# Optimization experiments

Hardware: AMD Instinct MI355X
Metric: run time of the kernel (lower is better)

Reference implementation:

```python
import jax, jax.numpy as jnp
import numpy as np

B, T, C, H = 4, 2048, 1024, 16
D = C // H  # head_size = 64


def setup_inputs() -> dict:
    key = jax.random.key(0)
    k1, k2, k3 = jax.random.split(key, 3)
    x = jax.random.normal(k1, (B, T, C), dtype=jnp.float32)
    w_qkv = jax.random.normal(k2, (C, 3 * C), dtype=jnp.float32) * (C ** -0.5)
    b_qkv = jnp.zeros((3 * C,), dtype=jnp.float32)
    w_proj = jax.random.normal(k3, (C, C), dtype=jnp.float32) * (C ** -0.5)
    b_proj = jnp.zeros((C,), dtype=jnp.float32)
    return {"x": x, "w_qkv": w_qkv, "b_qkv": b_qkv, "w_proj": w_proj, "b_proj": b_proj}


def reference(x, w_qkv, b_qkv, w_proj, b_proj):
    b, t, c = x.shape
    qkv = x @ w_qkv + b_qkv                      # [B,T,3C]
    q, k, v = jnp.split(qkv, 3, axis=-1)
    # [B,T,C] -> [B,H,T,D]
    q = q.reshape(b, t, H, D).transpose(0, 2, 1, 3)
    k = k.reshape(b, t, H, D).transpose(0, 2, 1, 3)
    v = v.reshape(b, t, H, D).transpose(0, 2, 1, 3)
    attn = jnp.einsum('bhqd,bhkd->bhqk', q, k) * (D ** -0.5)
    causal = jnp.tril(jnp.ones((t, t), dtype=bool))
    attn = jnp.where(causal[None, None], attn, -jnp.inf)
    attn = jax.nn.softmax(attn, axis=-1)
    # dropout: eval mode (identity)
    out = jnp.einsum('bhqk,bhkd->bhqd', attn, v)
    out = out.transpose(0, 2, 1, 3).reshape(b, t, c)
    return out @ w_proj + b_proj
```

## Files before the change

kernel.cpp:

```cpp
#include <hip/hip_runtime.h>

#define B_ 4
#define T_ 2048
#define C_ 1024
#define H_ 16
#define D_ 64

typedef __attribute__((ext_vector_type(8))) short short8;
typedef __attribute__((ext_vector_type(4))) float f32x4;

__device__ inline unsigned short f2bf(float f) {
    union { float f; unsigned u; } v; v.f = f;
    unsigned r = v.u + 0x7fffu + ((v.u >> 16) & 1u);
    return (unsigned short)(r >> 16);
}

__device__ inline unsigned int pk_bf16(float a, float b) {
#if __has_builtin(__builtin_amdgcn_cvt_pk_bf16_f32)
    typedef __attribute__((ext_vector_type(2))) __bf16 bf16x2;
    bf16x2 v = __builtin_amdgcn_cvt_pk_bf16_f32(a, b);
    return __builtin_bit_cast(unsigned int, v);
#else
    return (unsigned)f2bf(a) | ((unsigned)f2bf(b) << 16);
#endif
}

__device__ inline void async_ld16(const void* g, void* lds) {
    __builtin_amdgcn_global_load_lds(
        (const __attribute__((address_space(1))) unsigned int*)g,
        (__attribute__((address_space(3))) unsigned int*)lds, 16, 0, 0);
}

__global__ __launch_bounds__(256) void prep_all(
    const float* __restrict__ x, const float* __restrict__ w_qkv,
    const float* __restrict__ w_proj,
    unsigned short* __restrict__ xb, unsigned short* __restrict__ wqkvT,
    unsigned short* __restrict__ wprojT)
{
    const int bid = blockIdx.x;
    if (bid < 8192) {
        int i = (bid * 256 + threadIdx.x) * 4;
        float4 v = *(const float4*)(x + i);
        uint2 o;
        o.x = pk_bf16(v.x, v.y);
        o.y = pk_bf16(v.z, v.w);
        *(uint2*)(xb + i) = o;
        return;
    }
    __shared__ float tile[32][33];
    const int tt = bid - 8192;
    int bx = tt & 127;
    const int by = tt >> 7;
    const float* src; unsigned short* dst; int Cc;
    if (bx < 96) { src = w_qkv;  dst = wqkvT;  Cc = 3072; }
    else         { src = w_proj; dst = wprojT; Cc = 1024; bx -= 96; }
    const int tx = threadIdx.x & 31, ty = threadIdx.x >> 5;
    #pragma unroll
    for (int r = 0; r < 32; r += 8)
        tile[ty + r][tx] = src[(size_t)(by*32 + ty + r) * Cc + bx*32 + tx];
    __syncthreads();
    #pragma unroll
    for (int r = 0; r < 32; r += 8)
        dst[(size_t)(bx*32 + ty + r) * 1024 + by*32 + tx] = f2bf(tile[tx][ty + r]);
}

__global__ __launch_bounds__(256) void gemm_qkv(
    const unsigned short* __restrict__ A,
    const unsigned short* __restrict__ BT,
    const float* __restrict__ bias,
    unsigned short* __restrict__ qb, unsigned short* __restrict__ kb,
    unsigned short* __restrict__ vtb)
{
    __shared__ unsigned short As0[128 * 32], As1[128 * 32];
    __shared__ unsigned short Bs0[128 * 32], Bs1[128 * 32];
    const int tid = threadIdx.x;
    const int wave = tid >> 6, lane = tid & 63;
    const int wm = wave >> 1, wn = wave & 1;
    const int l15 = lane & 15, lq = lane >> 4;
    const int m0 = blockIdx.y * 128, n0 = blockIdx.x * 128;
    const int srow = tid >> 2, sg = tid & 3;
    const int sel = n0 >> 10;

    f32x4 acc[4][4] = {};

    for (int k0 = 0; k0 < 1024; k0 += 64) {
        #pragma unroll
        for (int r = 0; r < 2; ++r) {
            const size_t ra = (size_t)(m0 + r*64 + srow) * 1024 + k0 + sg*8;
            const size_t rb = (size_t)(n0 + r*64 + srow) * 1024 + k0 + sg*8;
            async_ld16(A  + ra,      (char*)As0 + r*4096 + wave*1024);
            async_ld16(A  + ra + 32, (char*)As1 + r*4096 + wave*1024);
            async_ld16(BT + rb,      (char*)Bs0 + r*4096 + wave*1024);
            async_ld16(BT + rb + 32, (char*)Bs1 + r*4096 + wave*1024);
        }
        __syncthreads();
        #pragma unroll
        for (int ks = 0; ks < 2; ++ks) {
            const unsigned short* Asx = ks ? As1 : As0;
            const unsigned short* Bsx = ks ? Bs1 : Bs0;
            short8 af[4], bf[4];
            #pragma unroll
            for (int i = 0; i < 4; ++i) {
                af[i] = *(const short8*)&Asx[(wm*64 + i*16 + l15) * 32 + lq*8];
                bf[i] = *(const short8*)&Bsx[(wn*64 + i*16 + l15) * 32 + lq*8];
            }
            if (sel < 2) {
                #pragma unroll
                for (int mi = 0; mi < 4; ++mi)
                    #pragma unroll
                    for (int ni = 0; ni < 4; ++ni)
                        acc[mi][ni] = __builtin_amdgcn_mfma_f32_16x16x32_bf16(
                            bf[ni], af[mi], acc[mi][ni], 0, 0, 0);
            } else {
                #pragma unroll
                for (int mi = 0; mi < 4; ++mi)
                    #pragma unroll
                    for (int ni = 0; ni < 4; ++ni)
                        acc[mi][ni] = __builtin_amdgcn_mfma_f32_16x16x32_bf16(
                            af[mi], bf[ni], acc[mi][ni], 0, 0, 0);
            }
        }
        __syncthreads();
    }

    if (sel < 2) {
        const float qs = (sel == 0) ? 0.180336880f : 1.0f;
        unsigned short* dst = (sel == 0) ? qb : kb;
        #pragma unroll
        for (int mi = 0; mi < 4; ++mi) {
            const int t = m0 + wm*64 + mi*16 + l15;
            const int bb = t >> 11, tt = t & 2047;
            #pragma unroll
            for (int ni = 0; ni < 4; ++ni) {
                const int nb = n0 + wn*64 + ni*16 + lq*4;
                const int hh = (nb >> 6) & 15, d0 = nb & 63;
                float4 bv = *(const float4*)(bias + nb);
                float v0 = (acc[mi][ni][0] + bv.x) * qs;
                float v1 = (acc[mi][ni][1] + bv.y) * qs;
                float v2 = (acc[mi][ni][2] + bv.z) * qs;
                float v3 = (acc[mi][ni][3] + bv.w) * qs;
                uint2 pk; pk.x = pk_bf16(v0, v1); pk.y = pk_bf16(v2, v3);
                *(uint2*)(dst + ((size_t)(bb*16 + hh)*2048 + tt)*64 + d0) = pk;
            }
        }
    } else {
        #pragma unroll
        for (int mi = 0; mi < 4; ++mi) {
            const int t0 = m0 + wm*64 + mi*16 + lq*4;
            const int bb = t0 >> 11, tt = t0 & 2047;
            const int tl = tt & 63;
            const int tp = (tt & ~63) | (tl & 32) | ((tl & 12) << 1) | ((tl & 16) >> 2);
            #pragma unroll
            for (int ni = 0; ni < 4; ++ni) {
                const int n = n0 + wn*64 + ni*16 + l15;
                const int hh = (n >> 6) & 15, d = n & 63;
                const float bs = bias[n];
                uint2 pk;
                pk.x = pk_bf16(acc[mi][ni][0] + bs, acc[mi][ni][1] + bs);
                pk.y = pk_bf16(acc[mi][ni][2] + bs, acc[mi][ni][3] + bs);
                *(uint2*)(vtb + ((size_t)(bb*16 + hh)*64 + d)*2048 + tp) = pk;
            }
        }
    }
}

__global__ __launch_bounds__(256) void gemm_proj(
    const unsigned short* __restrict__ A,
    const unsigned short* __restrict__ BT,
    const float* __restrict__ bias,
    float* __restrict__ out)
{
    __shared__ unsigned short As0[128 * 32], As1[128 * 32];
    __shared__ unsigned short Bs0[128 * 32], Bs1[128 * 32];
    const int tid = threadIdx.x;
    const int wave = tid >> 6, lane = tid & 63;
    const int wm = wave >> 1, wn = wave & 1;
    const int l15 = lane & 15, lq = lane >> 4;
    const int m0 = blockIdx.y * 128, n0 = blockIdx.x * 128;
    const int srow = tid >> 2, sg = tid & 3;

    f32x4 acc[4][4] = {};

    for (int k0 = 0; k0 < 1024; k0 += 64) {
        #pragma unroll
        for (int r = 0; r < 2; ++r) {
            const size_t ra = (size_t)(m0 + r*64 + srow) * 1024 + k0 + sg*8;
            const size_t rb = (size_t)(n0 + r*64 + srow) * 1024 + k0 + sg*8;
            async_ld16(A  + ra,      (char*)As0 + r*4096 + wave*1024);
            async_ld16(A  + ra + 32, (char*)As1 + r*4096 + wave*1024);
            async_ld16(BT + rb,      (char*)Bs0 + r*4096 + wave*1024);
            async_ld16(BT + rb + 32, (char*)Bs1 + r*4096 + wave*1024);
        }
        __syncthreads();
        #pragma unroll
        for (int ks = 0; ks < 2; ++ks) {
            const unsigned short* Asx = ks ? As1 : As0;
            const unsigned short* Bsx = ks ? Bs1 : Bs0;
            short8 af[4], bf[4];
            #pragma unroll
            for (int i = 0; i < 4; ++i) {
                af[i] = *(const short8*)&Asx[(wm*64 + i*16 + l15) * 32 + lq*8];
                bf[i] = *(const short8*)&Bsx[(wn*64 + i*16 + l15) * 32 + lq*8];
            }
            #pragma unroll
            for (int mi = 0; mi < 4; ++mi)
                #pragma unroll
                for (int ni = 0; ni < 4; ++ni)
                    acc[mi][ni] = __builtin_amdgcn_mfma_f32_16x16x32_bf16(
                        bf[ni], af[mi], acc[mi][ni], 0, 0, 0);
        }
        __syncthreads();
    }

    #pragma unroll
    for (int mi = 0; mi < 4; ++mi) {
        const int m = m0 + wm*64 + mi*16 + l15;
        #pragma unroll
        for (int ni = 0; ni < 4; ++ni) {
            const int nb = n0 + wn*64 + ni*16 + lq*4;
            float4 bv = *(const float4*)(bias + nb);
            float4 o;
            o.x = acc[mi][ni][0] + bv.x;
            o.y = acc[mi][ni][1] + bv.y;
            o.z = acc[mi][ni][2] + bv.z;
            o.w = acc[mi][ni][3] + bv.w;
            *(float4*)(out + (size_t)m * 1024 + nb) = o;
        }
    }
}

__global__ __launch_bounds__(256, 2) void attn_mfma(
    const unsigned short* __restrict__ qb,
    const unsigned short* __restrict__ kb,
    const unsigned short* __restrict__ vtb,
    unsigned short* __restrict__ ab)
{
    extern __shared__ unsigned char smem[];
    const int tid  = threadIdx.x;
    const int wave = tid >> 6, lane = tid & 63;
    const int l15  = lane & 15, lq = lane >> 4;
    const int linear = blockIdx.x;
    const int xc  = linear & 7;
    const int idx = linear >> 3;
    const int bh  = xc * 8 + (idx & 7);
    const int qblk = 31 - (idx >> 3);
    const int q0 = qblk * 64;
    const int b = bh >> 4, h = bh & 15;
    const size_t base = (size_t)bh * 2048 * 64;

    unsigned short* Kw = (unsigned short*)(smem + wave * 16384);
    unsigned short* Vw = Kw + 4096;

    const int row8 = lane >> 3;
    const int chx8 = ((lane & 7) ^ row8) * 8;

#define STAGE_K(J0) do { _Pragma("unroll") for (int op = 0; op < 8; ++op) \
    async_ld16(kb + base + (size_t)((J0) + op*8 + row8)*64 + chx8, \
               (char*)Kw + op*1024); } while (0)
#define STAGE_V(J0) do { _Pragma("unroll") for (int op = 0; op < 8; ++op) \
    async_ld16(vtb + base + (size_t)(op*8 + row8)*2048 + (J0) + chx8, \
               (char*)Vw + op*1024); } while (0)

    short8 qf[2][4];
    #pragma unroll
    for (int ks = 0; ks < 2; ++ks)
        #pragma unroll
        for (int nq = 0; nq < 4; ++nq)
            qf[ks][nq] = *(const short8*)(qb + base
                + (size_t)(q0 + nq*16 + l15)*64 + ks*32 + lq*8);

    f32x4 o[4][4] = {};
    float lacc[4] = {0.f, 0.f, 0.f, 0.f};

    const int jfirst = wave * 64;
    const int nt = (qblk >= wave) ? ((qblk - wave) >> 2) + 1 : 0;

    if (nt > 0) { STAGE_K(jfirst); STAGE_V(jfirst); }

    for (int i = 0; i < nt; ++i) {
        const int j0 = jfirst + i * 256;
        const bool more = (i + 1 < nt);

        asm volatile("s_waitcnt vmcnt(8)" ::: "memory");

        short8 kf0[4], kf1[4];
        #pragma unroll
        for (int ni = 0; ni < 4; ++ni) {
            const unsigned short* kr = Kw + (ni*16 + l15) * 64;
            kf0[ni] = *(const short8*)(kr + (((0*4 + lq) ^ (l15 & 7)) << 3));
            kf1[ni] = *(const short8*)(kr + (((1*4 + lq) ^ (l15 & 7)) << 3));
        }
        f32x4 s[4][4] = {};
        #pragma unroll
        for (int ni = 0; ni < 4; ++ni)
            #pragma unroll
            for (int nq = 0; nq < 4; ++nq) {
                s[ni][nq] = __builtin_amdgcn_mfma_f32_16x16x32_bf16(
                    kf0[ni], qf[0][nq], s[ni][nq], 0, 0, 0);
                s[ni][nq] = __builtin_amdgcn_mfma_f32_16x16x32_bf16(
                    kf1[ni], qf[1][nq], s[ni][nq], 0, 0, 0);
            }
        asm volatile("s_waitcnt lgkmcnt(0)" ::: "memory");
        if (more) STAGE_K(j0 + 256);

        if (j0 == q0) {
            #pragma unroll
            for (int ni = 0; ni < 4; ++ni)
                #pragma unroll
                for (int nq = 0; nq < 4; ++nq)
                    #pragma unroll
                    for (int r = 0; r < 4; ++r)
                        if (ni*16 + lq*4 + r > nq*16 + l15)
                            s[ni][nq][r] = -1e30f;
        }

        short8 pf[2][4];
        #pragma unroll
        for (int c = 0; c < 2; ++c)
            #pragma unroll
            for (int nq = 0; nq < 4; ++nq) {
                float p0 = __builtin_amdgcn_exp2f(s[2*c  ][nq][0]);
                float p1 = __builtin_amdgcn_exp2f(s[2*c  ][nq][1]);
                float p2 = __builtin_amdgcn_exp2f(s[2*c  ][nq][2]);
                float p3 = __builtin_amdgcn_exp2f(s[2*c  ][nq][3]);
                float p4 = __builtin_amdgcn_exp2f(s[2*c+1][nq][0]);
                float p5 = __builtin_amdgcn_exp2f(s[2*c+1][nq][1]);
                float p6 = __builtin_amdgcn_exp2f(s[2*c+1][nq][2]);
                float p7 = __builtin_amdgcn_exp2f(s[2*c+1][nq][3]);
                lacc[nq] += ((p0 + p1) + (p2 + p3)) + ((p4 + p5) + (p6 + p7));
                uint4 pu;
                pu.x = pk_bf16(p0, p1); pu.y = pk_bf16(p2, p3);
                pu.z = pk_bf16(p4, p5); pu.w = pk_bf16(p6, p7);
                pf[c][nq] = __builtin_bit_cast(short8, pu);
            }

        if (more) asm volatile("s_waitcnt vmcnt(8)" ::: "memory");
        else      asm volatile("s_waitcnt vmcnt(0)" ::: "memory");

        #pragma unroll
        for (int c = 0; c < 2; ++c) {
            short8 vf[4];
            #pragma unroll
            for (int nd = 0; nd < 4; ++nd)
                vf[nd] = *(const short8*)(Vw + (nd*16 + l15) * 64
                    + (((c*4 + lq) ^ (l15 & 7)) << 3));
            #pragma unroll
            for (int nq = 0; nq < 4; ++nq)
                #pragma unroll
                for (int nd = 0; nd < 4; ++nd)
                    o[nq][nd] = __builtin_amdgcn_mfma_f32_16x16x32_bf16(
                        pf[c][nq], vf[nd], o[nq][nd], 0, 0, 0);
        }
        asm volatile("s_waitcnt lgkmcnt(0)" ::: "memory");
        if (more) STAGE_V(j0 + 256);
    }
#undef STAGE_K
#undef STAGE_V

    #pragma unroll
    for (int nq = 0; nq < 4; ++nq) {
        float t = lacc[nq];
        t += __shfl_xor(t, 16);
        t += __shfl_xor(t, 32);
        if (lq == 0) ((float*)Kw)[nq*16 + l15] = t;
    }
    __syncthreads();
    const int qg = wave, d = lane;
    f32x4 linv4[4];
    #pragma unroll
    for (int j = 0; j < 4; ++j) {
        f32x4 lsum = {};
        #pragma unroll
        for (int w2 = 0; w2 < 4; ++w2)
            lsum += *(const f32x4*)((const float*)(smem + w2*16384) + qg*16 + j*4);
        #pragma unroll
        for (int r = 0; r < 4; ++r)
            linv4[j][r] = __builtin_amdgcn_rcpf(lsum[r]);
    }
    __syncthreads();
    #pragma unroll
    for (int nq = 0; nq < 4; ++nq)
        #pragma unroll
        for (int nd = 0; nd < 4; ++nd) {
            const int row = nd*16 + l15;
            const int col = (nq*16 + lq*4 + 4*l15) & 63;
            *(f32x4*)((float*)Kw + row*64 + col) = o[nq][nd];
        }
    __syncthreads();
    #pragma unroll
    for (int j = 0; j < 4; ++j) {
        const int colb = (qg*16 + j*4 + 4*(d & 15)) & 63;
        f32x4 acc = {};
        #pragma unroll
        for (int w2 = 0; w2 < 4; ++w2)
            acc += *(const f32x4*)((const float*)(smem + w2*16384) + d*64 + colb);
        #pragma unroll
        for (int r = 0; r < 4; ++r) {
            const int q = qg*16 + j*4 + r;
            ab[(size_t)(b*2048 + q0 + q)*1024 + h*64 + d] = f2bf(acc[r] * linv4[j][r]);
        }
    }
}

extern "C" void kernel_launch(void* const* d_in, const int* in_sizes, int n_in,
                              void* d_out, int out_size, void* d_ws, size_t ws_size,
                              hipStream_t stream) {
    const float* x      = (const float*)d_in[0];
    const float* w_qkv  = (const float*)d_in[1];
    const float* b_qkv  = (const float*)d_in[2];
    const float* w_proj = (const float*)d_in[3];
    const float* b_proj = (const float*)d_in[4];
    float* out = (float*)d_out;

    unsigned short* xb     = (unsigned short*)d_ws;
    unsigned short* wqkvT  = xb + 8388608;
    unsigned short* wprojT = wqkvT + 3145728;
    unsigned short* qbuf   = wprojT + 1048576;
    unsigned short* kbuf   = qbuf + 8388608;
    unsigned short* vtbuf  = kbuf + 8388608;
    unsigned short* abuf   = vtbuf + 8388608;

    prep_all<<<12288, 256, 0, stream>>>(x, w_qkv, w_proj, xb, wqkvT, wprojT);
    gemm_qkv<<<dim3(24, 64), 256, 0, stream>>>(xb, wqkvT, b_qkv, qbuf, kbuf, vtbuf);
    attn_mfma<<<2048, 256, 65536, stream>>>(qbuf, kbuf, vtbuf, abuf);
    gemm_proj<<<dim3(8, 64), 256, 0, stream>>>(abuf, wprojT, b_proj, out);
}
```

Baseline: 247.1 us.

## Swizzle GEMM LDS tiles and remap blocks for XCD-local L2 reuse

Both GEMM kernels now stage each 128x64 bf16 tile into a single XOR-swizzled LDS buffer, replacing the two split 32-column halves, so the MFMA fragment reads avoid bank conflicts. The launch grid is flattened to 1D and remapped so that consecutive blocks on the same XCD share M rows, improving L2 reuse of the A operand. The intent is to cut LDS bank conflicts and cross-XCD cache misses in the QKV and projection GEMMs. A macro alias for the MFMA builtin is cosmetic. The block-to-tile mapping assumes the grid sizes match exactly.

```diff
diff --git a/kernel.cpp b/kernel.cpp
--- a/kernel.cpp
+++ b/kernel.cpp
@@ -30,6 +30,8 @@
         (const __attribute__((address_space(1))) unsigned int*)g,
         (__attribute__((address_space(3))) unsigned int*)lds, 16, 0, 0);
 }
+
+#define MFMA_BF16 __builtin_amdgcn_mfma_f32_16x16x32_bf16
 
 __global__ __launch_bounds__(256) void prep_all(
     const float* __restrict__ x, const float* __restrict__ w_qkv,
@@ -71,53 +73,55 @@
     unsigned short* __restrict__ qb, unsigned short* __restrict__ kb,
     unsigned short* __restrict__ vtb)
 {
-    __shared__ unsigned short As0[128 * 32], As1[128 * 32];
-    __shared__ unsigned short Bs0[128 * 32], Bs1[128 * 32];
+    __shared__ unsigned short As[128 * 64];
+    __shared__ unsigned short Bs[128 * 64];
     const int tid = threadIdx.x;
     const int wave = tid >> 6, lane = tid & 63;
     const int wm = wave >> 1, wn = wave & 1;
     const int l15 = lane & 15, lq = lane >> 4;
-    const int m0 = blockIdx.y * 128, n0 = blockIdx.x * 128;
-    const int srow = tid >> 2, sg = tid & 3;
+    const int bid = blockIdx.x;
+    const int xcd = bid & 7, idx = bid >> 3;
+    const int m0 = (xcd * 8 + (idx & 7)) * 128;
+    const int n0 = (idx >> 3) * 128;
     const int sel = n0 >> 10;
+    const int row8 = lane >> 3;
+    const int chx8 = ((lane & 7) ^ row8) * 8;
+    const int cxa = l15 & 7;
 
     f32x4 acc[4][4] = {};
 
     for (int k0 = 0; k0 < 1024; k0 += 64) {
         #pragma unroll
-        for (int r = 0; r < 2; ++r) {
-            const size_t ra = (size_t)(m0 + r*64 + srow) * 1024 + k0 + sg*8;
-            const size_t rb = (size_t)(n0 + r*64 + srow) * 1024 + k0 + sg*8;
-            async_ld16(A  + ra,      (char*)As0 + r*4096 + wave*1024);
-            async_ld16(A  + ra + 32, (char*)As1 + r*4096 + wave*1024);
-            async_ld16(BT + rb,      (char*)Bs0 + r*4096 + wave*1024);
-            async_ld16(BT + rb + 32, (char*)Bs1 + r*4096 + wave*1024);
+        for (int c = 0; c < 4; ++c) {
+            const int r = wave*32 + c*8;
+            async_ld16(A  + (size_t)(m0 + r + row8)*1024 + k0 + chx8,
+                       (char*)As + r*128);
+            async_ld16(BT + (size_t)(n0 + r + row8)*1024 + k0 + chx8,
+                       (char*)Bs + r*128);
         }
         __syncthreads();
         #pragma unroll
         for (int ks = 0; ks < 2; ++ks) {
-            const unsigned short* Asx = ks ? As1 : As0;
-            const unsigned short* Bsx = ks ? Bs1 : Bs0;
             short8 af[4], bf[4];
             #pragma unroll
             for (int i = 0; i < 4; ++i) {
-                af[i] = *(const short8*)&Asx[(wm*64 + i*16 + l15) * 32 + lq*8];
-                bf[i] = *(const short8*)&Bsx[(wn*64 + i*16 + l15) * 32 + lq*8];
+                const int ra = wm*64 + i*16 + l15;
+                const int rb = wn*64 + i*16 + l15;
+                af[i] = *(const short8*)&As[ra*64 + (((ks*4 + lq) ^ cxa) << 3)];
+                bf[i] = *(const short8*)&Bs[rb*64 + (((ks*4 + lq) ^ cxa) << 3)];
             }
             if (sel < 2) {
                 #pragma unroll
                 for (int mi = 0; mi < 4; ++mi)
                     #pragma unroll
                     for (int ni = 0; ni < 4; ++ni)
-                        acc[mi][ni] = __builtin_amdgcn_mfma_f32_16x16x32_bf16(
-                            bf[ni], af[mi], acc[mi][ni], 0, 0, 0);
+                        acc[mi][ni] = MFMA_BF16(bf[ni], af[mi], acc[mi][ni], 0, 0, 0);
             } else {
                 #pragma unroll
                 for (int mi = 0; mi < 4; ++mi)
                     #pragma unroll
                     for (int ni = 0; ni < 4; ++ni)
-                        acc[mi][ni] = __builtin_amdgcn_mfma_f32_16x16x32_bf16(
-                            af[mi], bf[ni], acc[mi][ni], 0, 0, 0);
+                        acc[mi][ni] = MFMA_BF16(af[mi], bf[ni], acc[mi][ni], 0, 0, 0);
             }
         }
         __syncthreads();
@@ -170,44 +174,47 @@
     const float* __restrict__ bias,
     float* __restrict__ out)
 {
-    __shared__ unsigned short As0[128 * 32], As1[128 * 32];
-    __shared__ unsigned short Bs0[128 * 32], Bs1[128 * 32];
+    __shared__ unsigned short As[128 * 64];
+    __shared__ unsigned short Bs[128 * 64];
     const int tid = threadIdx.x;
     const int wave = tid >> 6, lane = tid & 63;
     const int wm = wave >> 1, wn = wave & 1;
     const int l15 = lane & 15, lq = lane >> 4;
-    const int m0 = blockIdx.y * 128, n0 = blockIdx.x * 128;
-    const int srow = tid >> 2, sg = tid & 3;
+    const int bid = blockIdx.x;
+    const int xcd = bid & 7, idx = bid >> 3;
+    const int m0 = (xcd * 8 + (idx & 7)) * 128;
+    const int n0 = (idx >> 3) * 128;
+    const int row8 = lane >> 3;
+    const int chx8 = ((lane & 7) ^ row8) * 8;
+    const int cxa = l15 & 7;
 
     f32x4 acc[4][4] = {};
 
     for (int k0 = 0; k0 < 1024; k0 += 64) {
         #pragma unroll
-        for (int r = 0; r < 2; ++r) {
-            const size_t ra = (size_t)(m0 + r*64 + srow) * 1024 + k0 + sg*8;
-            const size_t rb = (size_t)(n0 + r*64 + srow) * 1024 + k0 + sg*8;
-            async_ld16(A  + ra,      (char*)As0 + r*4096 + wave*1024);
-            async_ld16(A  + ra + 32, (char*)As1 + r*4096 + wave*1024);
-            async_ld16(BT + rb,      (char*)Bs0 + r*4096 + wave*1024);
-            async_ld16(BT + rb + 32, (char*)Bs1 + r*4096 + wave*1024);
+        for (int c = 0; c < 4; ++c) {
+            const int r = wave*32 + c*8;
+            async_ld16(A  + (size_t)(m0 + r + row8)*1024 + k0 + chx8,
+                       (char*)As + r*128);
+            async_ld16(BT + (size_t)(n0 + r + row8)*1024 + k0 + chx8,
+                       (char*)Bs + r*128);
         }
         __syncthreads();
         #pragma unroll
         for (int ks = 0; ks < 2; ++ks) {
-            const unsigned short* Asx = ks ? As1 : As0;
-            const unsigned short* Bsx = ks ? Bs1 : Bs0;
             short8 af[4], bf[4];
             #pragma unroll
             for (int i = 0; i < 4; ++i) {
-                af[i] = *(const short8*)&Asx[(wm*64 + i*16 + l15) * 32 + lq*8];
-                bf[i] = *(const short8*)&Bsx[(wn*64 + i*16 + l15) * 32 + lq*8];
+                const int ra = wm*64 + i*16 + l15;
+                const int rb = wn*64 + i*16 + l15;
+                af[i] = *(const short8*)&As[ra*64 + (((ks*4 + lq) ^ cxa) << 3)];
+                bf[i] = *(const short8*)&Bs[rb*64 + (((ks*4 + lq) ^ cxa) << 3)];
             }
             #pragma unroll
             for (int mi = 0; mi < 4; ++mi)
                 #pragma unroll
                 for (int ni = 0; ni < 4; ++ni)
-                    acc[mi][ni] = __builtin_amdgcn_mfma_f32_16x16x32_bf16(
-                        bf[ni], af[mi], acc[mi][ni], 0, 0, 0);
+                    acc[mi][ni] = MFMA_BF16(bf[ni], af[mi], acc[mi][ni], 0, 0, 0);
         }
         __syncthreads();
     }
@@ -295,10 +302,8 @@
         for (int ni = 0; ni < 4; ++ni)
             #pragma unroll
             for (int nq = 0; nq < 4; ++nq) {
-                s[ni][nq] = __builtin_amdgcn_mfma_f32_16x16x32_bf16(
-                    kf0[ni], qf[0][nq], s[ni][nq], 0, 0, 0);
-                s[ni][nq] = __builtin_amdgcn_mfma_f32_16x16x32_bf16(
-                    kf1[ni], qf[1][nq], s[ni][nq], 0, 0, 0);
+                s[ni][nq] = MFMA_BF16(kf0[ni], qf[0][nq], s[ni][nq], 0, 0, 0);
+                s[ni][nq] = MFMA_BF16(kf1[ni], qf[1][nq], s[ni][nq], 0, 0, 0);
             }
         asm volatile("s_waitcnt lgkmcnt(0)" ::: "memory");
         if (more) STAGE_K(j0 + 256);
@@ -348,8 +353,7 @@
             for (int nq = 0; nq < 4; ++nq)
                 #pragma unroll
                 for (int nd = 0; nd < 4; ++nd)
-                    o[nq][nd] = __builtin_amdgcn_mfma_f32_16x16x32_bf16(
-                        pf[c][nq], vf[nd], o[nq][nd], 0, 0, 0);
+                    o[nq][nd] = MFMA_BF16(pf[c][nq], vf[nd], o[nq][nd], 0, 0, 0);
         }
         asm volatile("s_waitcnt lgkmcnt(0)" ::: "memory");
         if (more) STAGE_V(j0 + 256);
@@ -421,7 +425,7 @@
     unsigned short* abuf   = vtbuf + 8388608;
 
     prep_all<<<12288, 256, 0, stream>>>(x, w_qkv, w_proj, xb, wqkvT, wprojT);
-    gemm_qkv<<<dim3(24, 64), 256, 0, stream>>>(xb, wqkvT, b_qkv, qbuf, kbuf, vtbuf);
+    gemm_qkv<<<1536, 256, 0, stream>>>(xb, wqkvT, b_qkv, qbuf, kbuf, vtbuf);
     attn_mfma<<<2048, 256, 65536, stream>>>(qbuf, kbuf, vtbuf, abuf);
-    gemm_proj<<<dim3(8, 64), 256, 0, stream>>>(abuf, wprojT, b_proj, out);
-}
+    gemm_proj<<<512, 256, 0, stream>>>(abuf, wprojT, b_proj, out);
+}
```

Result: faster. 239.0 us (-3.3%).
